# Performance work log

Hardware: AMD Instinct MI355X
Metric: run time of the kernel (lower is better)

The kernel has to match this reference:

```python
import jax, jax.numpy as jnp
import numpy as np

EPS = 1e-6
BASE_TAU = 1.0  # temperature, learnable_tau=False


def setup_inputs() -> dict:
    key = jax.random.key(0)
    k1, k2, k3 = jax.random.split(key, 3)
    n, b, t, h = 16, 4, 2048, 1024
    num_blocks = 24
    return {
        "values": jax.random.normal(k1, (n, b, t, h), dtype=jnp.float32),
        "w_query": jax.random.normal(k2, (num_blocks, h), dtype=jnp.float32) * 0.02,
        "key_pos_bias": jax.random.normal(k3, (num_blocks, h), dtype=jnp.float32) * 0.02,
        "position": 16,
    }


def reference(values, w_query, key_pos_bias, position):
    # values: [n, b, t, h] stacked completed block outputs, n == position
    fp = values.astype(jnp.float32)
    # weight-free RMSNorm (BlockAttnRes._rms_norm)
    inv = jax.lax.rsqrt(jnp.mean(fp * fp, axis=-1, keepdims=True) + EPS)
    keys = fp * inv
    # positional bias for the first `position` block slots
    keys = keys + key_pos_bias[:position].astype(keys.dtype)[:, None, None, :]
    query = w_query[position].astype(jnp.float32)  # [h]
    scale = jnp.sqrt(jnp.float32(values.shape[-1])) * BASE_TAU
    scores = jnp.einsum('h,nbth->nbt', query, keys) / scale  # [n, b, t]
    alpha = jax.nn.softmax(scores, axis=0)                    # softmax over history n
    routed = jnp.einsum('nbt,nbth->bth', alpha, fp).astype(values.dtype)
    alpha_bth = jnp.transpose(alpha, (1, 2, 0))               # [b, t, n]
    return routed, alpha_bth
```

## Files before the change

kernel.cpp:

```cpp
#include <hip/hip_runtime.h>
#include <math.h>

#define H     1024
#define NBLK  16
#define BT    8192
#define ROUTED_SIZE (BT * H)
#define SCALE_INV (1.0f / 32.0f)

typedef float v4f __attribute__((ext_vector_type(4)));

__global__ __launch_bounds__(1024) void qb_kernel(
    const float* __restrict__ w_query,
    const float* __restrict__ key_pos_bias,
    const int*   __restrict__ pos_p,
    float*       __restrict__ qb)
{
    const int n    = threadIdx.x >> 6;
    const int lane = threadIdx.x & 63;
    const int pos  = *pos_p;

    const float* q = w_query      + (size_t)pos * H;
    const float* b = key_pos_bias + (size_t)n   * H;

    float s = 0.0f;
#pragma unroll
    for (int j = 0; j < 4; ++j) {
        const int h = lane * 16 + j * 4;
        const float4 qv = *(const float4*)(q + h);
        const float4 bv = *(const float4*)(b + h);
        s += qv.x * bv.x + qv.y * bv.y + qv.z * bv.z + qv.w * bv.w;
    }
#pragma unroll
    for (int off = 32; off; off >>= 1) s += __shfl_xor(s, off, 64);
    if (lane == 0) qb[n] = s;
}

__global__ __launch_bounds__(1024, 8) void block_attn_res_kernel(
    const float* __restrict__ values,
    const float* __restrict__ w_query,
    const int*   __restrict__ pos_p,
    const float* __restrict__ qb,
    float*       __restrict__ out)
{
    const int bt  = blockIdx.x;
    const int tid = threadIdx.x;
    const int c   = tid & 255;
    const int g   = tid >> 8;
    const int h0  = c << 2;

    __shared__ float2 pv[NBLK][256];
    __shared__ v4f    rp[4][256];
    __shared__ float  scores[NBLK];

    const int pos = *pos_p;
    const v4f q = *(const v4f*)(w_query + (size_t)pos * H + h0);

    v4f v[4];
    const float* vbase = values + (size_t)bt * H + h0 + (size_t)g * 4 * BT * H;
#pragma unroll
    for (int i = 0; i < 4; ++i)
        v[i] = *(const v4f*)(vbase + (size_t)i * BT * H);

#pragma unroll
    for (int i = 0; i < 4; ++i) {
        const v4f x  = v[i];
        const v4f xx = x * x;
        const v4f qx = q * x;
        pv[g * 4 + i][c] = make_float2((xx[0] + xx[1]) + (xx[2] + xx[3]),
                                       (qx[0] + qx[1]) + (qx[2] + qx[3]));
    }
    __syncthreads();

    {
        const int n2   = tid >> 6;
        const int lane = tid & 63;
        const float2 p0 = pv[n2][lane];
        const float2 p1 = pv[n2][lane + 64];
        const float2 p2 = pv[n2][lane + 128];
        const float2 p3 = pv[n2][lane + 192];
        float ss = (p0.x + p1.x) + (p2.x + p3.x);
        float qv = (p0.y + p1.y) + (p2.y + p3.y);
#pragma unroll
        for (int off = 32; off; off >>= 1) {
            ss += __shfl_xor(ss, off, 64);
            qv += __shfl_xor(qv, off, 64);
        }
        if (lane == 0) {
            const float inv = rsqrtf(ss * (1.0f / (float)H) + 1e-6f);
            scores[n2] = (inv * qv + qb[n2]) * SCALE_INV;
        }
    }
    __syncthreads();

    float m = -3.402823466e38f;
#pragma unroll
    for (int n = 0; n < NBLK; ++n) m = fmaxf(m, scores[n]);

    float ag[4];
    float sum = 0.0f;
#pragma unroll
    for (int n = 0; n < NBLK; ++n) {
        const float e = __expf(scores[n] - m);
        sum += e;
        if ((n >> 2) == g) ag[n & 3] = e;
    }
    const float rs = 1.0f / sum;

    v4f acc = {0.0f, 0.0f, 0.0f, 0.0f};
#pragma unroll
    for (int i = 0; i < 4; ++i) acc += (ag[i] * rs) * v[i];
    rp[g][c] = acc;
    __syncthreads();

    if (g == 0) {
        const v4f r = (rp[0][c] + rp[1][c]) + (rp[2][c] + rp[3][c]);
        __builtin_nontemporal_store(r, (v4f*)(out + (size_t)bt * H + h0));
    }

    if (tid < NBLK)
        out[(size_t)ROUTED_SIZE + (size_t)bt * NBLK + tid]
            = __expf(scores[tid] - m) * rs;
}

extern "C" void kernel_launch(void* const* d_in, const int* in_sizes, int n_in,
                              void* d_out, int out_size, void* d_ws, size_t ws_size,
                              hipStream_t stream) {
    const float* values       = (const float*)d_in[0];
    const float* w_query      = (const float*)d_in[1];
    const float* key_pos_bias = (const float*)d_in[2];
    const int*   position     = (const int*)d_in[3];
    float*       out          = (float*)d_out;
    float*       qb           = (float*)d_ws;

    hipLaunchKernelGGL(qb_kernel, dim3(1), dim3(1024), 0, stream,
                       w_query, key_pos_bias, position, qb);
    hipLaunchKernelGGL(block_attn_res_kernel, dim3(BT), dim3(1024), 0, stream,
                       values, w_query, position, qb, out);
}
```

Measured before the change: 682.8 us.

## Process four bt columns per block with all loads issued upfront

Each block now handles four consecutive bt positions and issues all 16 vector loads up front, so more memory traffic is in flight per thread before any reduction starts. The softmax is recomputed by one 16-lane group using shuffles and broadcast through shared memory. __syncthreads is replaced by a custom lgkmcnt-wait plus s_barrier. Register use rises (64 floats of values per thread), the minimum-occupancy launch bound is dropped, and each column adds more barriers, which may cut occupancy.

```diff
diff --git a/kernel.cpp b/kernel.cpp
--- a/kernel.cpp
+++ b/kernel.cpp
@@ -6,8 +6,11 @@
 #define BT    8192
 #define ROUTED_SIZE (BT * H)
 #define SCALE_INV (1.0f / 32.0f)
+#define TCOLS 4
 
 typedef float v4f __attribute__((ext_vector_type(4)));
+
+#define BAR() asm volatile("s_waitcnt lgkmcnt(0)\n\ts_barrier" ::: "memory")
 
 __global__ __launch_bounds__(1024) void qb_kernel(
     const float* __restrict__ w_query,
@@ -35,91 +38,99 @@
     if (lane == 0) qb[n] = s;
 }
 
-__global__ __launch_bounds__(1024, 8) void block_attn_res_kernel(
+__global__ __launch_bounds__(1024) void block_attn_res_kernel(
     const float* __restrict__ values,
     const float* __restrict__ w_query,
     const int*   __restrict__ pos_p,
     const float* __restrict__ qb,
     float*       __restrict__ out)
 {
-    const int bt  = blockIdx.x;
     const int tid = threadIdx.x;
     const int c   = tid & 255;
     const int g   = tid >> 8;
     const int h0  = c << 2;
+    const int bt0 = blockIdx.x * TCOLS;
 
     __shared__ float2 pv[NBLK][256];
     __shared__ v4f    rp[4][256];
     __shared__ float  scores[NBLK];
+    __shared__ float  alf[NBLK];
+
+    v4f v[TCOLS][4];
+    const float* base = values + (size_t)(g * 4) * BT * H + (size_t)bt0 * H + h0;
+#pragma unroll
+    for (int j = 0; j < TCOLS; ++j)
+#pragma unroll
+        for (int i = 0; i < 4; ++i)
+            v[j][i] = *(const v4f*)(base + (size_t)i * BT * H + (size_t)j * H);
 
     const int pos = *pos_p;
     const v4f q = *(const v4f*)(w_query + (size_t)pos * H + h0);
 
-    v4f v[4];
-    const float* vbase = values + (size_t)bt * H + h0 + (size_t)g * 4 * BT * H;
 #pragma unroll
-    for (int i = 0; i < 4; ++i)
-        v[i] = *(const v4f*)(vbase + (size_t)i * BT * H);
+    for (int j = 0; j < TCOLS; ++j) {
+        const size_t bt = (size_t)bt0 + j;
 
 #pragma unroll
-    for (int i = 0; i < 4; ++i) {
-        const v4f x  = v[i];
-        const v4f xx = x * x;
-        const v4f qx = q * x;
-        pv[g * 4 + i][c] = make_float2((xx[0] + xx[1]) + (xx[2] + xx[3]),
-                                       (qx[0] + qx[1]) + (qx[2] + qx[3]));
+        for (int i = 0; i < 4; ++i) {
+            const v4f x  = v[j][i];
+            const v4f xx = x * x;
+            const v4f qx = q * x;
+            pv[g * 4 + i][c] = make_float2((xx[0] + xx[1]) + (xx[2] + xx[3]),
+                                           (qx[0] + qx[1]) + (qx[2] + qx[3]));
+        }
+        BAR();
+
+        {
+            const int w    = tid >> 6;
+            const int lane = tid & 63;
+            const float2 p0 = pv[w][lane];
+            const float2 p1 = pv[w][lane + 64];
+            const float2 p2 = pv[w][lane + 128];
+            const float2 p3 = pv[w][lane + 192];
+            float ss = (p0.x + p1.x) + (p2.x + p3.x);
+            float qv = (p0.y + p1.y) + (p2.y + p3.y);
+#pragma unroll
+            for (int off = 32; off; off >>= 1) {
+                ss += __shfl_xor(ss, off, 64);
+                qv += __shfl_xor(qv, off, 64);
+            }
+            if (lane == 0) {
+                const float inv = rsqrtf(ss * (1.0f / (float)H) + 1e-6f);
+                scores[w] = (inv * qv + qb[w]) * SCALE_INV;
+            }
+        }
+        BAR();
+
+        if (tid < NBLK) {
+            const float s = scores[tid];
+            float mx = s;
+#pragma unroll
+            for (int off = 1; off <= 8; off <<= 1)
+                mx = fmaxf(mx, __shfl_xor(mx, off, 64));
+            const float e = __expf(s - mx);
+            float sm = e;
+#pragma unroll
+            for (int off = 1; off <= 8; off <<= 1)
+                sm += __shfl_xor(sm, off, 64);
+            const float a = e / sm;
+            alf[tid] = a;
+            out[(size_t)ROUTED_SIZE + bt * NBLK + tid] = a;
+        }
+        BAR();
+
+        {
+            const float a0 = alf[4 * g], a1 = alf[4 * g + 1];
+            const float a2 = alf[4 * g + 2], a3 = alf[4 * g + 3];
+            rp[g][c] = a0 * v[j][0] + a1 * v[j][1] + a2 * v[j][2] + a3 * v[j][3];
+        }
+        BAR();
+        if (g == 0) {
+            const v4f r = (rp[0][c] + rp[1][c]) + (rp[2][c] + rp[3][c]);
+            __builtin_nontemporal_store(r, (v4f*)(out + bt * H + h0));
+        }
+        if (j + 1 < TCOLS) BAR();
     }
-    __syncthreads();
-
-    {
-        const int n2   = tid >> 6;
-        const int lane = tid & 63;
-        const float2 p0 = pv[n2][lane];
-        const float2 p1 = pv[n2][lane + 64];
-        const float2 p2 = pv[n2][lane + 128];
-        const float2 p3 = pv[n2][lane + 192];
-        float ss = (p0.x + p1.x) + (p2.x + p3.x);
-        float qv = (p0.y + p1.y) + (p2.y + p3.y);
-#pragma unroll
-        for (int off = 32; off; off >>= 1) {
-            ss += __shfl_xor(ss, off, 64);
-            qv += __shfl_xor(qv, off, 64);
-        }
-        if (lane == 0) {
-            const float inv = rsqrtf(ss * (1.0f / (float)H) + 1e-6f);
-            scores[n2] = (inv * qv + qb[n2]) * SCALE_INV;
-        }
-    }
-    __syncthreads();
-
-    float m = -3.402823466e38f;
-#pragma unroll
-    for (int n = 0; n < NBLK; ++n) m = fmaxf(m, scores[n]);
-
-    float ag[4];
-    float sum = 0.0f;
-#pragma unroll
-    for (int n = 0; n < NBLK; ++n) {
-        const float e = __expf(scores[n] - m);
-        sum += e;
-        if ((n >> 2) == g) ag[n & 3] = e;
-    }
-    const float rs = 1.0f / sum;
-
-    v4f acc = {0.0f, 0.0f, 0.0f, 0.0f};
-#pragma unroll
-    for (int i = 0; i < 4; ++i) acc += (ag[i] * rs) * v[i];
-    rp[g][c] = acc;
-    __syncthreads();
-
-    if (g == 0) {
-        const v4f r = (rp[0][c] + rp[1][c]) + (rp[2][c] + rp[3][c]);
-        __builtin_nontemporal_store(r, (v4f*)(out + (size_t)bt * H + h0));
-    }
-
-    if (tid < NBLK)
-        out[(size_t)ROUTED_SIZE + (size_t)bt * NBLK + tid]
-            = __expf(scores[tid] - m) * rs;
 }
 
 extern "C" void kernel_launch(void* const* d_in, const int* in_sizes, int n_in,
@@ -134,6 +145,6 @@
 
     hipLaunchKernelGGL(qb_kernel, dim3(1), dim3(1024), 0, stream,
                        w_query, key_pos_bias, position, qb);
-    hipLaunchKernelGGL(block_attn_res_kernel, dim3(BT), dim3(1024), 0, stream,
+    hipLaunchKernelGGL(block_attn_res_kernel, dim3(BT / TCOLS), dim3(1024), 0, stream,
                        values, w_query, position, qb, out);
 }
```

Result: slower. 717.4 us (+5.1%).
